# Optimization experiments

Measured on AMD Instinct MI355X. Metric: run time of the kernel, lower is better.

The kernel has to match this reference:

```python
import jax, jax.numpy as jnp
import numpy as np

B, D_MODEL, HIDEEN, HEAD, IMG_H, IMG_W = 16, 512, 512, 8, 32, 32
D_K = D_MODEL // HEAD
EPS = 1e-5


def setup_inputs() -> dict:
    key = jax.random.key(0)
    ks = jax.random.split(key, 9)
    s_in = 1.0 / np.sqrt(D_MODEL)
    s_h = 1.0 / np.sqrt(HIDEEN)
    return {
        "x": jax.random.normal(ks[0], (B, D_MODEL, IMG_H, IMG_W), jnp.float32),
        "Wq": jax.random.uniform(ks[1], (HIDEEN, D_MODEL), jnp.float32, -s_in, s_in),
        "bq": jax.random.uniform(ks[2], (HIDEEN,), jnp.float32, -s_in, s_in),
        "Wk": jax.random.uniform(ks[3], (HIDEEN, D_MODEL), jnp.float32, -s_in, s_in),
        "bk": jax.random.uniform(ks[4], (HIDEEN,), jnp.float32, -s_in, s_in),
        "Wv": jax.random.uniform(ks[5], (HIDEEN, D_MODEL), jnp.float32, -s_in, s_in),
        "bv": jax.random.uniform(ks[6], (HIDEEN,), jnp.float32, -s_in, s_in),
        "Wo": jax.random.uniform(ks[7], (HIDEEN, HIDEEN), jnp.float32, -s_h, s_h),
        "bo": jax.random.uniform(ks[8], (HIDEEN,), jnp.float32, -s_h, s_h),
    }


def _conv1x1(x, W, b):
    # x: [B, Cin, H, W], W: [Cout, Cin]
    return jnp.einsum("bchw,oc->bohw", x, W) + b[None, :, None, None]


def _heads(t):
    # torch: [B, C, H, W] -> view(B, -1, head, d_k) -> transpose(1, 2)
    return t.reshape(B, -1, HEAD, D_K).transpose(0, 2, 1, 3)  # [B, head, N, d_k]


def reference(x, Wq, bq, Wk, bk, Wv, bv, Wo, bo):
    q = _heads(_conv1x1(x, Wq, bq))
    k = _heads(_conv1x1(x, Wk, bk))
    v = _heads(_conv1x1(x, Wv, bv))
    scores = jnp.einsum("bhnd,bhmd->bhnm", q, k) / np.sqrt(D_K).astype(np.float32)
    attn = jax.nn.softmax(scores, axis=-1)
    out = jnp.einsum("bhnm,bhmd->bhnd", attn, v)  # [B, head, N, d_k]
    # back to image layout: [B, N, head*d_k] -> [B, hideen, H, W]
    out = out.transpose(0, 2, 1, 3).reshape(B, -1, HEAD * D_K)
    out = out.transpose(0, 2, 1).reshape(B, -1, IMG_H, IMG_W)
    out = _conv1x1(out, Wo, bo)
    # InstanceNorm2d (affine=False, biased var, eps=1e-5)
    mu = out.mean(axis=(2, 3), keepdims=True)
    var = out.var(axis=(2, 3), keepdims=True)
    out = (out - mu) / jnp.sqrt(var + EPS)
    # original applies the SAME attn_out conv a second time
    out = _conv1x1(out, Wo, bo)
    return out
```

## Files before the change

kernel.cpp:

```cpp
#include <hip/hip_runtime.h>


typedef short bf16x8_t __attribute__((ext_vector_type(8)));
typedef float f32x4_t  __attribute__((ext_vector_type(4)));

union U4 {
  uint4 u;
  bf16x8_t v;
  unsigned short us[8];
};

__device__ __forceinline__ unsigned short f2bf(float f) {
  union { float f; unsigned int u; } x; x.f = f;
  unsigned int r = x.u + 0x7fffu + ((x.u >> 16) & 1u);
  return (unsigned short)(r >> 16);
}

#define BATCH_STRIDE (512 * 1024)

__global__ __launch_bounds__(256) void cvtx_k(
    const float* __restrict__ x, unsigned short* __restrict__ xb)
{
  __shared__ float tile[32][33];
  const int b = blockIdx.z, c0 = blockIdx.y * 32, n0 = blockIdx.x * 32;
  const int t = threadIdx.x;
  {
    const int cl_ = t >> 3, n4 = (t & 7) * 4;
    const float4 u = *(const float4*)(x + (size_t)b * BATCH_STRIDE
                                      + (size_t)(c0 + cl_) * 1024 + n0 + n4);
    tile[cl_][n4] = u.x; tile[cl_][n4 + 1] = u.y;
    tile[cl_][n4 + 2] = u.z; tile[cl_][n4 + 3] = u.w;
  }
  __syncthreads();
  {
    const int nl = t >> 3, c4 = (t & 7) * 4;
    ushort4 o;
    o.x = f2bf(tile[c4][nl]);     o.y = f2bf(tile[c4 + 1][nl]);
    o.z = f2bf(tile[c4 + 2][nl]); o.w = f2bf(tile[c4 + 3][nl]);
    *(ushort4*)(xb + (size_t)b * BATCH_STRIDE + (size_t)(n0 + nl) * 512
                + c0 + c4) = o;
  }
}

template<int OUTF>
__device__ __forceinline__ void gemm_core(
    const float* __restrict__ W, const float* __restrict__ bias,
    const unsigned short* __restrict__ src, void* __restrict__ dst,
    int m0, int n0, int b, unsigned short* sA, unsigned short* sB)
{
  const int t = threadIdx.x;
  const int lane = t & 63, wv = t >> 6, qd = lane >> 4, cl = lane & 15;
  const int wm = wv >> 1, wn = wv & 1;
  const unsigned short* srcb = src + (size_t)b * BATCH_STRIDE + (size_t)n0 * 512;

  f32x4_t acc[4][4];
  #pragma unroll
  for (int i = 0; i < 4; ++i)
    #pragma unroll
    for (int f = 0; f < 4; ++f) acc[i][f] = (f32x4_t){0.f, 0.f, 0.f, 0.f};

  const int ar = t >> 2, akf = (t & 3) * 8;

  for (int kk = 0; kk < 512; kk += 32) {
    if (kk) __syncthreads();
    #pragma unroll
    for (int p = 0; p < 2; ++p) {
      const int row = p * 64 + ar;
      const float* wr = W + (size_t)(m0 + row) * 512 + kk + akf;
      const float4 w0 = *(const float4*)wr;
      const float4 w1 = *(const float4*)(wr + 4);
      U4 wa;
      wa.us[0] = f2bf(w0.x); wa.us[1] = f2bf(w0.y);
      wa.us[2] = f2bf(w0.z); wa.us[3] = f2bf(w0.w);
      wa.us[4] = f2bf(w1.x); wa.us[5] = f2bf(w1.y);
      wa.us[6] = f2bf(w1.z); wa.us[7] = f2bf(w1.w);
      *(uint4*)(sA + row * 40 + akf) = wa.u;
      *(uint4*)(sB + row * 40 + akf) =
          *(const uint4*)(srcb + (size_t)row * 512 + kk + akf);
    }
    __syncthreads();
    U4 af[4], bf[4];
    #pragma unroll
    for (int i = 0; i < 4; ++i) {
      af[i].u = *(const uint4*)(sA + (wm * 64 + i * 16 + cl) * 40 + qd * 8);
      bf[i].u = *(const uint4*)(sB + (wn * 64 + i * 16 + cl) * 40 + qd * 8);
    }
    #pragma unroll
    for (int i = 0; i < 4; ++i)
      #pragma unroll
      for (int f = 0; f < 4; ++f)
        acc[i][f] = __builtin_amdgcn_mfma_f32_16x16x32_bf16(
            af[i].v, bf[f].v, acc[i][f], 0, 0, 0);
  }

  #pragma unroll
  for (int i = 0; i < 4; ++i) {
    #pragma unroll
    for (int r = 0; r < 4; ++r) {
      const int o = m0 + wm * 64 + i * 16 + qd * 4 + r;
      const float bv = bias[o];
      #pragma unroll
      for (int f = 0; f < 4; ++f) {
        const int n = n0 + wn * 64 + f * 16 + cl;
        const size_t idx = (size_t)b * BATCH_STRIDE + (size_t)o * 1024 + n;
        const float val = acc[i][f][r] + bv;
        if (OUTF) ((float*)dst)[idx] = val;
        else      ((unsigned short*)dst)[idx] = f2bf(val);
      }
    }
  }
}

struct QKVArgs {
  const float* W[3];
  const float* bias[3];
  unsigned short* dst[3];
};

__global__ __launch_bounds__(256) void qkv_k(
    QKVArgs args, const unsigned short* __restrict__ xb)
{
  __shared__ __align__(16) unsigned short sA[128 * 40];
  __shared__ __align__(16) unsigned short sB[128 * 40];
  const int widx = blockIdx.y >> 2;
  const int m0 = (blockIdx.y & 3) * 128;
  gemm_core<0>(args.W[widx], args.bias[widx], xb, args.dst[widx],
               m0, blockIdx.x * 128, blockIdx.z, sA, sB);
}

template<int OUTF>
__global__ __launch_bounds__(256) void gemm_wo_k(
    const float* __restrict__ W, const float* __restrict__ bias,
    const unsigned short* __restrict__ src, void* __restrict__ dst)
{
  __shared__ __align__(16) unsigned short sA[128 * 40];
  __shared__ __align__(16) unsigned short sB[128 * 40];
  gemm_core<OUTF>(W, bias, src, dst, blockIdx.y * 128, blockIdx.x * 128,
                  blockIdx.z, sA, sB);
}

__global__ __launch_bounds__(256) void attn_k(
    const unsigned short* __restrict__ Q,
    const unsigned short* __restrict__ K,
    const unsigned short* __restrict__ V,
    unsigned short* __restrict__ O)
{
  __shared__ __align__(16) unsigned short sK[64 * 72];
  __shared__ __align__(16) unsigned short sV[64 * 72];
  __shared__ __align__(16) unsigned short sP[4 * 16 * 72];

  const int t = threadIdx.x;
  const int lane = t & 63, wv = t >> 6, qd = lane >> 4, cl = lane & 15;
  const int b = blockIdx.y >> 3, h = blockIdx.y & 7;
  const int i0 = blockIdx.x * 64;
  const size_t bbase = (size_t)b * BATCH_STRIDE;
  const int hoff = h * 64;

  U4 aq0, aq1;
  {
    const unsigned short* qp =
        Q + bbase + (size_t)(i0 + wv * 16 + cl) * 512 + hoff + qd * 8;
    aq0.u = *(const uint4*)qp;
    aq1.u = *(const uint4*)(qp + 32);
  }

  f32x4_t oacc[4];
  #pragma unroll
  for (int f = 0; f < 4; ++f) oacc[f] = (f32x4_t){0.f, 0.f, 0.f, 0.f};
  float rs[4] = {0.f, 0.f, 0.f, 0.f};

  for (int j0 = 0; j0 < 1024; j0 += 64) {
    __syncthreads();
    #pragma unroll
    for (int p = 0; p < 2; ++p) {
      const int ki = p * 32 + (t >> 3), kd0 = (t & 7) * 8;
      *(uint4*)(sK + ki * 72 + kd0) =
          *(const uint4*)(K + bbase + (size_t)(j0 + ki) * 512 + hoff + kd0);
    }
    #pragma unroll
    for (int p = 0; p < 2; ++p) {
      const int vi = t & 63, vd0 = (t >> 6) * 8 + p * 32;
      U4 u; u.u = *(const uint4*)(V + bbase + (size_t)(j0 + vi) * 512 + hoff + vd0);
      #pragma unroll
      for (int j = 0; j < 8; ++j) sV[(vd0 + j) * 72 + vi] = u.us[j];
    }
    __syncthreads();

    f32x4_t s[4];
    #pragma unroll
    for (int nh = 0; nh < 4; ++nh) {
      s[nh] = (f32x4_t){0.f, 0.f, 0.f, 0.f};
      U4 bk0; bk0.u = *(const uint4*)(sK + (nh * 16 + cl) * 72 + qd * 8);
      U4 bk1; bk1.u = *(const uint4*)(sK + (nh * 16 + cl) * 72 + 32 + qd * 8);
      s[nh] = __builtin_amdgcn_mfma_f32_16x16x32_bf16(aq0.v, bk0.v, s[nh], 0, 0, 0);
      s[nh] = __builtin_amdgcn_mfma_f32_16x16x32_bf16(aq1.v, bk1.v, s[nh], 0, 0, 0);
    }

    #pragma unroll
    for (int nh = 0; nh < 4; ++nh) {
      #pragma unroll
      for (int r = 0; r < 4; ++r) {
        const float pv = __expf(s[nh][r] * 0.125f);
        sP[wv * 1152 + (qd * 4 + r) * 72 + nh * 16 + cl] = f2bf(pv);
        rs[r] += pv;
      }
    }

    __syncthreads();

    U4 pf0, pf1;
    pf0.u = *(const uint4*)(sP + wv * 1152 + cl * 72 + qd * 8);
    pf1.u = *(const uint4*)(sP + wv * 1152 + cl * 72 + 32 + qd * 8);
    #pragma unroll
    for (int f = 0; f < 4; ++f) {
      U4 vf0, vf1;
      vf0.u = *(const uint4*)(sV + (f * 16 + cl) * 72 + qd * 8);
      vf1.u = *(const uint4*)(sV + (f * 16 + cl) * 72 + 32 + qd * 8);
      oacc[f] = __builtin_amdgcn_mfma_f32_16x16x32_bf16(pf0.v, vf0.v, oacc[f], 0, 0, 0);
      oacc[f] = __builtin_amdgcn_mfma_f32_16x16x32_bf16(pf1.v, vf1.v, oacc[f], 0, 0, 0);
    }
  }

  #pragma unroll
  for (int m = 1; m < 16; m <<= 1)
    #pragma unroll
    for (int r = 0; r < 4; ++r) rs[r] += __shfl_xor(rs[r], m);

  #pragma unroll
  for (int f = 0; f < 4; ++f) {
    #pragma unroll
    for (int r = 0; r < 4; ++r) {
      const int i = i0 + wv * 16 + qd * 4 + r;
      const int j = hoff + f * 16 + cl;
      O[bbase + (size_t)i * 512 + j] = f2bf(oacc[f][r] / rs[r]);
    }
  }
}

__global__ __launch_bounds__(256) void norm_k(
    const float* __restrict__ x, unsigned short* __restrict__ y)
{
  __shared__ float tile[8][1028];
  __shared__ float shm[8], shv[8];
  const int b = blockIdx.x >> 6, c0 = (blockIdx.x & 63) * 8;
  const int t = threadIdx.x;
  const int ch = t >> 5, ln = t & 31;
  const float* xr = x + (size_t)b * BATCH_STRIDE + (size_t)(c0 + ch) * 1024;
  float s1 = 0.f, s2 = 0.f;
  #pragma unroll
  for (int j = 0; j < 8; ++j) {
    const int n = ln * 4 + j * 128;
    const float4 u = *(const float4*)(xr + n);
    tile[ch][n] = u.x; tile[ch][n + 1] = u.y;
    tile[ch][n + 2] = u.z; tile[ch][n + 3] = u.w;
    s1 += u.x + u.y + u.z + u.w;
    s2 += u.x * u.x + u.y * u.y + u.z * u.z + u.w * u.w;
  }
  #pragma unroll
  for (int m = 1; m < 32; m <<= 1) {
    s1 += __shfl_xor(s1, m);
    s2 += __shfl_xor(s2, m);
  }
  if (ln == 0) {
    const float mean = s1 * (1.f / 1024.f);
    const float var = s2 * (1.f / 1024.f) - mean * mean;
    shm[ch] = mean;
    shv[ch] = rsqrtf(var + 1e-5f);
  }
  __syncthreads();
  unsigned short* yb = y + (size_t)b * BATCH_STRIDE;
  #pragma unroll
  for (int jn = 0; jn < 4; ++jn) {
    const int n = t + jn * 256;
    U4 o;
    #pragma unroll
    for (int c = 0; c < 8; ++c)
      o.us[c] = f2bf((tile[c][n] - shm[c]) * shv[c]);
    *(uint4*)(yb + (size_t)n * 512 + c0) = o.u;
  }
}

extern "C" void kernel_launch(void* const* d_in, const int* in_sizes, int n_in,
                              void* d_out, int out_size, void* d_ws, size_t ws_size,
                              hipStream_t stream) {
  const float* x  = (const float*)d_in[0];
  const float* Wq = (const float*)d_in[1];
  const float* bq = (const float*)d_in[2];
  const float* Wk = (const float*)d_in[3];
  const float* bk = (const float*)d_in[4];
  const float* Wv = (const float*)d_in[5];
  const float* bv = (const float*)d_in[6];
  const float* Wo = (const float*)d_in[7];
  const float* bo = (const float*)d_in[8];

  const size_t BUF = (size_t)16 * BATCH_STRIDE;
  unsigned short* xb = (unsigned short*)d_ws;
  unsigned short* Qb = xb + BUF;
  unsigned short* Kb = Qb + BUF;
  unsigned short* Vb = (unsigned short*)d_out;
  unsigned short* Ob = Vb + BUF;
  float*          out1f = (float*)d_ws;
  unsigned short* out1n = Kb;

  QKVArgs qa;
  qa.W[0] = Wq; qa.W[1] = Wk; qa.W[2] = Wv;
  qa.bias[0] = bq; qa.bias[1] = bk; qa.bias[2] = bv;
  qa.dst[0] = Qb; qa.dst[1] = Kb; qa.dst[2] = Vb;

  cvtx_k<<<dim3(32, 16, 16), 256, 0, stream>>>(x, xb);
  qkv_k<<<dim3(8, 12, 16), 256, 0, stream>>>(qa, xb);
  attn_k<<<dim3(16, 128), 256, 0, stream>>>(Qb, Kb, Vb, Ob);
  gemm_wo_k<1><<<dim3(8, 4, 16), 256, 0, stream>>>(Wo, bo, Ob, out1f);
  norm_k<<<dim3(16 * 64), 256, 0, stream>>>(out1f, out1n);
  gemm_wo_k<1><<<dim3(8, 4, 16), 256, 0, stream>>>(Wo, bo, out1n, d_out);
}
```

Baseline: 292.3 us.

## Pre-transpose V in a separate kernel and remap attention blocks per XCD

Adds a transpose kernel that writes V as [b][channel][token] into the free xb buffer. The attention kernel can then load V tiles with vectorized 16-byte copies instead of eight scalar transposed LDS stores per thread. The attention block index is also remapped so that the 16 query blocks of one (batch, head) land on the same XCD, which should improve L2 reuse of K and V. The cost is one extra kernel launch and an extra read and write pass over V.

```diff
diff --git a/kernel.cpp b/kernel.cpp
--- a/kernel.cpp
+++ b/kernel.cpp
@@ -139,10 +139,32 @@
                   blockIdx.z, sA, sB);
 }
 
+__global__ __launch_bounds__(256) void vt_k(
+    const unsigned short* __restrict__ src, unsigned short* __restrict__ dst)
+{
+  __shared__ unsigned short tile[32][36];
+  const int b = blockIdx.z, j0 = blockIdx.y * 32, p0 = blockIdx.x * 32;
+  const int t = threadIdx.x;
+  {
+    const int pr = t >> 3, jc = (t & 7) * 4;
+    *(ushort4*)&tile[pr][jc] = *(const ushort4*)(
+        src + (size_t)b * BATCH_STRIDE + (size_t)(p0 + pr) * 512 + j0 + jc);
+  }
+  __syncthreads();
+  {
+    const int jr = t >> 3, pc = (t & 7) * 4;
+    ushort4 o;
+    o.x = tile[pc][jr];     o.y = tile[pc + 1][jr];
+    o.z = tile[pc + 2][jr]; o.w = tile[pc + 3][jr];
+    *(ushort4*)(dst + (size_t)b * BATCH_STRIDE + (size_t)(j0 + jr) * 1024
+                + p0 + pc) = o;
+  }
+}
+
 __global__ __launch_bounds__(256) void attn_k(
     const unsigned short* __restrict__ Q,
     const unsigned short* __restrict__ K,
-    const unsigned short* __restrict__ V,
+    const unsigned short* __restrict__ Vt,
     unsigned short* __restrict__ O)
 {
   __shared__ __align__(16) unsigned short sK[64 * 72];
@@ -151,8 +173,13 @@
 
   const int t = threadIdx.x;
   const int lane = t & 63, wv = t >> 6, qd = lane >> 4, cl = lane & 15;
-  const int b = blockIdx.y >> 3, h = blockIdx.y & 7;
-  const int i0 = blockIdx.x * 64;
+
+  const int g = blockIdx.y * 16 + blockIdx.x;
+  const int xcd = g & 7, rest = g >> 3;
+  const int iblk = rest & 15;
+  const int bh = (rest >> 4) * 8 + xcd;
+  const int b = bh >> 3, h = bh & 7;
+  const int i0 = iblk * 64;
   const size_t bbase = (size_t)b * BATCH_STRIDE;
   const int hoff = h * 64;
 
@@ -173,16 +200,11 @@
     __syncthreads();
     #pragma unroll
     for (int p = 0; p < 2; ++p) {
-      const int ki = p * 32 + (t >> 3), kd0 = (t & 7) * 8;
-      *(uint4*)(sK + ki * 72 + kd0) =
-          *(const uint4*)(K + bbase + (size_t)(j0 + ki) * 512 + hoff + kd0);
-    }
-    #pragma unroll
-    for (int p = 0; p < 2; ++p) {
-      const int vi = t & 63, vd0 = (t >> 6) * 8 + p * 32;
-      U4 u; u.u = *(const uint4*)(V + bbase + (size_t)(j0 + vi) * 512 + hoff + vd0);
-      #pragma unroll
-      for (int j = 0; j < 8; ++j) sV[(vd0 + j) * 72 + vi] = u.us[j];
+      const int row = p * 32 + (t >> 3), c8 = (t & 7) * 8;
+      *(uint4*)(sK + row * 72 + c8) =
+          *(const uint4*)(K + bbase + (size_t)(j0 + row) * 512 + hoff + c8);
+      *(uint4*)(sV + row * 72 + c8) =
+          *(const uint4*)(Vt + bbase + (size_t)(hoff + row) * 1024 + j0 + c8);
     }
     __syncthreads();
 
@@ -299,6 +321,7 @@
   unsigned short* Kb = Qb + BUF;
   unsigned short* Vb = (unsigned short*)d_out;
   unsigned short* Ob = Vb + BUF;
+  unsigned short* Vt = xb;
   float*          out1f = (float*)d_ws;
   unsigned short* out1n = Kb;
 
@@ -309,7 +332,8 @@
 
   cvtx_k<<<dim3(32, 16, 16), 256, 0, stream>>>(x, xb);
   qkv_k<<<dim3(8, 12, 16), 256, 0, stream>>>(qa, xb);
-  attn_k<<<dim3(16, 128), 256, 0, stream>>>(Qb, Kb, Vb, Ob);
+  vt_k<<<dim3(32, 16, 16), 256, 0, stream>>>(Vb, Vt);
+  attn_k<<<dim3(16, 128), 256, 0, stream>>>(Qb, Kb, Vt, Ob);
   gemm_wo_k<1><<<dim3(8, 4, 16), 256, 0, stream>>>(Wo, bo, Ob, out1f);
   norm_k<<<dim3(16 * 64), 256, 0, stream>>>(out1f, out1n);
   gemm_wo_k<1><<<dim3(8, 4, 16), 256, 0, stream>>>(Wo, bo, out1n, d_out);
```

After: 278.9 us. -4.6%, faster.
